# Kernel optimization log

Measured on AMD Instinct MI355X. Metric: run time of the kernel, lower is better.

The kernel has to match this reference:

```python
import jax, jax.numpy as jnp
import numpy as np

MARGIN = 1.0


def setup_inputs() -> dict:
    key = jax.random.key(0)
    k1, k2 = jax.random.split(key)
    N, D = 512, 128
    inp = jax.random.normal(k1, (N, D), dtype=jnp.float32)
    tgt = jax.random.randint(k2, (N,), 0, 32, dtype=jnp.int64)
    return {"input": inp, "target": tgt}


def reference(input, target):
    emb = input.astype(jnp.float32)                      # [N, d]
    N = emb.shape[0]
    # --- pairwise squared distances (note: original never takes sqrt) ---
    sq = jnp.sum(emb * emb, axis=-1)                     # [N]
    pdist = sq[:, None] + sq[None, :] - 2.0 * (emb @ emb.T)
    pdist = jnp.maximum(pdist, 0.0)
    # error_mask (pdist>0 -> 1 else 0) then multiply == identity after clamp;
    # zero the diagonal as in mask_offdiagonals
    pdist = pdist * (1.0 - jnp.eye(N, dtype=pdist.dtype))  # [N, N]

    adjacency = target[:, None] == target[None, :]       # [N, N] bool
    adjacency_not = ~adjacency

    # --- semi-hard negative mining ---
    # mask3[i, j, k] = (label[k] != label[i]) & (D[i,k] > D[i,j])
    # (faithful to the O(N^3) tile in the torch code, expressed as a broadcast)
    mask3 = adjacency_not[:, None, :] & (pdist[:, None, :] > pdist[:, :, None])
    mask3_f = mask3.astype(jnp.float32)                  # [N, N, N]
    mask_final = jnp.any(mask3, axis=2)                  # [N, N]

    # masked min trick: min((D - rowmax) * mask) + rowmax
    row_max = jnp.max(pdist, axis=1, keepdims=True)      # [N, 1]
    negatives_outside = (
        jnp.min((pdist[:, None, :] - row_max[:, :, None]) * mask3_f, axis=2)
        + row_max
    )                                                    # [N, N]

    # masked max trick over all negatives: max((D - rowmin) * adj_not) + rowmin
    row_min = jnp.min(pdist, axis=1, keepdims=True)      # [N, 1]
    negatives_inside = (
        jnp.max((pdist - row_min) * adjacency_not.astype(jnp.float32),
                axis=1, keepdims=True)
        + row_min
    )                                                    # [N, 1] -> broadcast

    semi_hard_negatives = jnp.where(mask_final, negatives_outside, negatives_inside)

    loss_mat = MARGIN + pdist - semi_hard_negatives
    mask_positives = adjacency.astype(jnp.float32) - jnp.eye(N, dtype=jnp.float32)
    num_positives = jnp.sum(mask_positives)
    triplet_loss = jnp.sum(jnp.maximum(loss_mat * mask_positives, 0.0)) / num_positives
    return triplet_loss.astype(input.dtype)
```

## Files before the change

### kernel.cpp

```cpp
#include <hip/hip_runtime.h>

#define N_PTS 512
#define DIM 128
#define F4_PER_ROW 32
#define TLMARGIN 1.0f

__global__ __launch_bounds__(512)
void k_rows(const float* __restrict__ inp,
            const int* __restrict__ tgt,
            float2* __restrict__ rl) {
  const int i0 = blockIdx.x * 2;
  const int tid = threadIdx.x;
  const int lane = tid & 63;
  const int wave = tid >> 6;
  const int G = tid >> 3;
  const int s = tid & 7;

  __shared__ float d[2][N_PTS];
  __shared__ int lab[N_PTS];
  __shared__ float red[32];
  __shared__ unsigned long long pm0[8];
  __shared__ unsigned long long pm1[8];
  __shared__ int plist0[N_PTS];
  __shared__ int plist1[N_PTS];

  lab[tid] = tgt[tid];

  const float4* inp4 = reinterpret_cast<const float4*>(inp);

  float4 a0f[4], a1f[4];
  float sa0 = 0.f, sa1 = 0.f;
#pragma unroll
  for (int q = 0; q < 4; ++q) {
    a0f[q] = inp4[i0 * F4_PER_ROW + q * 8 + s];
    a1f[q] = inp4[(i0 + 1) * F4_PER_ROW + q * 8 + s];
    sa0 += a0f[q].x * a0f[q].x + a0f[q].y * a0f[q].y + a0f[q].z * a0f[q].z + a0f[q].w * a0f[q].w;
    sa1 += a1f[q].x * a1f[q].x + a1f[q].y * a1f[q].y + a1f[q].z * a1f[q].z + a1f[q].w * a1f[q].w;
  }
#pragma unroll
  for (int off = 1; off <= 4; off <<= 1) {
    sa0 += __shfl_xor(sa0, off);
    sa1 += __shfl_xor(sa1, off);
  }

#pragma unroll 2
  for (int r = 0; r < 8; ++r) {
    const int j = r * 64 + G;
    float dot0 = 0.f, dot1 = 0.f, sj = 0.f;
#pragma unroll
    for (int q = 0; q < 4; ++q) {
      const float4 bv = inp4[j * F4_PER_ROW + q * 8 + s];
      dot0 += a0f[q].x * bv.x + a0f[q].y * bv.y + a0f[q].z * bv.z + a0f[q].w * bv.w;
      dot1 += a1f[q].x * bv.x + a1f[q].y * bv.y + a1f[q].z * bv.z + a1f[q].w * bv.w;
      sj   += bv.x * bv.x + bv.y * bv.y + bv.z * bv.z + bv.w * bv.w;
    }
#pragma unroll
    for (int off = 1; off <= 4; off <<= 1) {
      dot0 += __shfl_xor(dot0, off);
      dot1 += __shfl_xor(dot1, off);
      sj   += __shfl_xor(sj, off);
    }
    if (s == 0) {
      float pd0 = fmaxf(sa0 + sj - 2.0f * dot0, 0.0f);
      float pd1 = fmaxf(sa1 + sj - 2.0f * dot1, 0.0f);
      if (j == i0) pd0 = 0.0f;
      if (j == i0 + 1) pd1 = 0.0f;
      d[0][j] = pd0;
      d[1][j] = pd1;
    }
  }
  __syncthreads();

  const int li0 = lab[i0];
  const int li1 = lab[i0 + 1];

  const float d0t = d[0][tid];
  const float d1t = d[1][tid];
  float nm0 = (lab[tid] != li0) ? d0t : 0.0f;
  float nm1 = (lab[tid] != li1) ? d1t : 0.0f;
#pragma unroll
  for (int off = 32; off; off >>= 1) {
    nm0 = fmaxf(nm0, __shfl_xor(nm0, off));
    nm1 = fmaxf(nm1, __shfl_xor(nm1, off));
  }
  const bool isPos0 = (lab[tid] == li0) && (tid != i0);
  const bool isPos1 = (lab[tid] == li1) && (tid != i0 + 1);
  const unsigned long long m0 = __ballot(isPos0);
  const unsigned long long m1 = __ballot(isPos1);
  if (lane == 0) {
    red[wave] = nm0;
    red[8 + wave] = nm1;
    pm0[wave] = m0;
    pm1[wave] = m1;
  }
  __syncthreads();

  float negin0 = red[0], negin1 = red[8];
#pragma unroll
  for (int w = 1; w < 8; ++w) {
    negin0 = fmaxf(negin0, red[w]);
    negin1 = fmaxf(negin1, red[8 + w]);
  }

  int P0 = 0, rank0 = 0, P1 = 0, rank1 = 0;
#pragma unroll
  for (int w = 0; w < 8; ++w) {
    const int c0 = __popcll(pm0[w]);
    const int c1 = __popcll(pm1[w]);
    if (w < wave) { rank0 += c0; rank1 += c1; }
    P0 += c0;
    P1 += c1;
  }
  rank0 += __popcll(pm0[wave] & ((1ull << lane) - 1ull));
  rank1 += __popcll(pm1[wave] & ((1ull << lane) - 1ull));
  if (isPos0) plist0[rank0] = tid;
  if (isPos1) plist1[rank1] = tid;
  __syncthreads();

  float ls0 = 0.0f, pc0 = 0.0f, ls1 = 0.0f, pc1 = 0.0f;
  for (int p = wave; p < P0; p += 8) {
    const int j = plist0[p];
    const float dj = d[0][j];
    float mn = __builtin_inff();
#pragma unroll
    for (int kk = 0; kk < N_PTS / 64; ++kk) {
      const int k = lane + (kk << 6);
      const float dk = d[0][k];
      if (lab[k] != li0 && dk > dj) mn = fminf(mn, dk);
    }
#pragma unroll
    for (int off = 32; off; off >>= 1) mn = fminf(mn, __shfl_xor(mn, off));
    const float shn = (mn < __builtin_inff()) ? mn : negin0;
    ls0 += fmaxf(TLMARGIN + dj - shn, 0.0f);
    pc0 += 1.0f;
  }
  for (int p = wave; p < P1; p += 8) {
    const int j = plist1[p];
    const float dj = d[1][j];
    float mn = __builtin_inff();
#pragma unroll
    for (int kk = 0; kk < N_PTS / 64; ++kk) {
      const int k = lane + (kk << 6);
      const float dk = d[1][k];
      if (lab[k] != li1 && dk > dj) mn = fminf(mn, dk);
    }
#pragma unroll
    for (int off = 32; off; off >>= 1) mn = fminf(mn, __shfl_xor(mn, off));
    const float shn = (mn < __builtin_inff()) ? mn : negin1;
    ls1 += fmaxf(TLMARGIN + dj - shn, 0.0f);
    pc1 += 1.0f;
  }

  if (lane == 0) {
    red[wave] = ls0;
    red[8 + wave] = pc0;
    red[16 + wave] = ls1;
    red[24 + wave] = pc1;
  }
  __syncthreads();
  if (tid == 0) {
    float a = 0.f, b = 0.f, c = 0.f, e = 0.f;
#pragma unroll
    for (int w = 0; w < 8; ++w) {
      a += red[w];
      b += red[8 + w];
      c += red[16 + w];
      e += red[24 + w];
    }
    rl[i0] = make_float2(a, b);
    rl[i0 + 1] = make_float2(c, e);
  }
}

__global__ __launch_bounds__(256)
void k_reduce(const float2* __restrict__ rl, float* __restrict__ out) {
  __shared__ float red[8];
  const int tid = threadIdx.x;
  const float2 a = rl[tid];
  const float2 b = rl[tid + 256];
  float l = a.x + b.x;
  float c = a.y + b.y;
#pragma unroll
  for (int off = 32; off; off >>= 1) {
    l += __shfl_xor(l, off);
    c += __shfl_xor(c, off);
  }
  const int lane = tid & 63, wave = tid >> 6;
  if (lane == 0) { red[wave] = l; red[4 + wave] = c; }
  __syncthreads();
  if (tid == 0) {
    float L = 0.0f, C = 0.0f;
#pragma unroll
    for (int w = 0; w < 4; ++w) { L += red[w]; C += red[4 + w]; }
    out[0] = L / C;
  }
}

extern "C" void kernel_launch(void* const* d_in, const int* in_sizes, int n_in,
                              void* d_out, int out_size, void* d_ws, size_t ws_size,
                              hipStream_t stream) {
  const float* inp = (const float*)d_in[0];
  const int* tgt = (const int*)d_in[1];
  float* out = (float*)d_out;

  float2* rl = (float2*)d_ws;

  k_rows<<<N_PTS / 2, 512, 0, stream>>>(inp, tgt, rl);
  k_reduce<<<1, 256, 0, stream>>>(rl, out);
}
```

Measured before the change: 16.00 us.

## Replace reduce kernel with per-block atomic accumulation and class-count positive totals

Drops the second reduction kernel. Each block now works out the global positive-pair count from per-class label histograms in shared memory, divides its partial loss by that count, and atomically adds the result to the output, which is zeroed by a memset beforehand. This removes one kernel launch and the workspace round trip, but adds a memset operation, 256 float atomics on one address, and a nondeterministic summation order. The histogram assumes labels fall in [0,32).

```diff
diff --git a/kernel.cpp b/kernel.cpp
--- a/kernel.cpp
+++ b/kernel.cpp
@@ -3,12 +3,13 @@
 #define N_PTS 512
 #define DIM 128
 #define F4_PER_ROW 32
+#define NCLASS 32
 #define TLMARGIN 1.0f
 
 __global__ __launch_bounds__(512)
 void k_rows(const float* __restrict__ inp,
             const int* __restrict__ tgt,
-            float2* __restrict__ rl) {
+            float* __restrict__ out) {
   const int i0 = blockIdx.x * 2;
   const int tid = threadIdx.x;
   const int lane = tid & 63;
@@ -18,12 +19,14 @@
 
   __shared__ float d[2][N_PTS];
   __shared__ int lab[N_PTS];
+  __shared__ int cnt[NCLASS];
   __shared__ float red[32];
   __shared__ unsigned long long pm0[8];
   __shared__ unsigned long long pm1[8];
   __shared__ int plist0[N_PTS];
   __shared__ int plist1[N_PTS];
 
+  if (tid < NCLASS) cnt[tid] = 0;
   lab[tid] = tgt[tid];
 
   const float4* inp4 = reinterpret_cast<const float4*>(inp);
@@ -71,6 +74,8 @@
   }
   __syncthreads();
 
+  atomicAdd(&cnt[lab[tid]], 1);
+
   const int li0 = lab[i0];
   const int li1 = lab[i0 + 1];
 
@@ -117,7 +122,7 @@
   if (isPos1) plist1[rank1] = tid;
   __syncthreads();
 
-  float ls0 = 0.0f, pc0 = 0.0f, ls1 = 0.0f, pc1 = 0.0f;
+  float ls0 = 0.0f, ls1 = 0.0f;
   for (int p = wave; p < P0; p += 8) {
     const int j = plist0[p];
     const float dj = d[0][j];
@@ -132,7 +137,6 @@
     for (int off = 32; off; off >>= 1) mn = fminf(mn, __shfl_xor(mn, off));
     const float shn = (mn < __builtin_inff()) ? mn : negin0;
     ls0 += fmaxf(TLMARGIN + dj - shn, 0.0f);
-    pc0 += 1.0f;
   }
   for (int p = wave; p < P1; p += 8) {
     const int j = plist1[p];
@@ -148,51 +152,21 @@
     for (int off = 32; off; off >>= 1) mn = fminf(mn, __shfl_xor(mn, off));
     const float shn = (mn < __builtin_inff()) ? mn : negin1;
     ls1 += fmaxf(TLMARGIN + dj - shn, 0.0f);
-    pc1 += 1.0f;
   }
 
   if (lane == 0) {
     red[wave] = ls0;
-    red[8 + wave] = pc0;
     red[16 + wave] = ls1;
-    red[24 + wave] = pc1;
   }
   __syncthreads();
   if (tid == 0) {
-    float a = 0.f, b = 0.f, c = 0.f, e = 0.f;
+    float a = 0.f;
 #pragma unroll
-    for (int w = 0; w < 8; ++w) {
-      a += red[w];
-      b += red[8 + w];
-      c += red[16 + w];
-      e += red[24 + w];
-    }
-    rl[i0] = make_float2(a, b);
-    rl[i0 + 1] = make_float2(c, e);
-  }
-}
-
-__global__ __launch_bounds__(256)
-void k_reduce(const float2* __restrict__ rl, float* __restrict__ out) {
-  __shared__ float red[8];
-  const int tid = threadIdx.x;
-  const float2 a = rl[tid];
-  const float2 b = rl[tid + 256];
-  float l = a.x + b.x;
-  float c = a.y + b.y;
+    for (int w = 0; w < 8; ++w) a += red[w] + red[16 + w];
+    int C = 0;
 #pragma unroll
-  for (int off = 32; off; off >>= 1) {
-    l += __shfl_xor(l, off);
-    c += __shfl_xor(c, off);
-  }
-  const int lane = tid & 63, wave = tid >> 6;
-  if (lane == 0) { red[wave] = l; red[4 + wave] = c; }
-  __syncthreads();
-  if (tid == 0) {
-    float L = 0.0f, C = 0.0f;
-#pragma unroll
-    for (int w = 0; w < 4; ++w) { L += red[w]; C += red[4 + w]; }
-    out[0] = L / C;
+    for (int k = 0; k < NCLASS; ++k) C += cnt[k] * (cnt[k] - 1);
+    atomicAdd(out, a / (float)C);
   }
 }
 
@@ -203,8 +177,6 @@
   const int* tgt = (const int*)d_in[1];
   float* out = (float*)d_out;
 
-  float2* rl = (float2*)d_ws;
-
-  k_rows<<<N_PTS / 2, 512, 0, stream>>>(inp, tgt, rl);
-  k_reduce<<<1, 256, 0, stream>>>(rl, out);
+  hipMemsetAsync(out, 0, sizeof(float), stream);
+  k_rows<<<N_PTS / 2, 512, 0, stream>>>(inp, tgt, out);
 }
```

New measurement: 20.73 us. 1.3x slower.
